# Kernel tuning notes

Hardware: AMD Instinct MI355X
Metric: run time of the kernel (lower is better)

Reference implementation:

```python
import jax, jax.numpy as jnp
import numpy as np

NUM_HEADS = 16

def setup_inputs() -> dict:
    key = jax.random.key(0)
    k1, k2, k3 = jax.random.split(key, 3)
    B, N, C = 2, 2048, 1024
    x = jax.random.normal(k1, (B, N, C), dtype=jnp.float32)
    w_qkv = jax.random.normal(k2, (C, 3 * C), dtype=jnp.float32) * (C ** -0.5)
    w_proj = jax.random.normal(k3, (C, C), dtype=jnp.float32) * (C ** -0.5)
    b_proj = jnp.zeros((C,), dtype=jnp.float32)
    return {"x": x, "w_qkv": w_qkv, "w_proj": w_proj, "b_proj": b_proj}

def reference(x, w_qkv, w_proj, b_proj):
    B, N, C = x.shape
    H = NUM_HEADS
    D = C // H
    scale = D ** -0.5
    qkv = x @ w_qkv                               # [B,N,3C]
    qkv = qkv.reshape(B, N, 3, H, D).transpose(2, 0, 3, 1, 4)  # [3,B,H,N,D]
    q, k, v = qkv[0] * scale, qkv[1], qkv[2]
    attn = jnp.einsum('bhnd,bhmd->bhnm', q, k)    # [B,H,N,N]
    attn = jax.nn.softmax(attn, axis=-1)
    out = jnp.einsum('bhnm,bhmd->bhnd', attn, v)  # [B,H,N,D]
    out = out.transpose(0, 2, 1, 3).reshape(B, N, C)
    return out @ w_proj + b_proj
```

## Files before the change

### kernel.cpp

```cpp
#include <hip/hip_runtime.h>

typedef unsigned short ushort_t;
typedef __attribute__((ext_vector_type(8))) short short8;
typedef __attribute__((ext_vector_type(4))) float f32x4;

#define AS1 __attribute__((address_space(1)))
#define AS3 __attribute__((address_space(3)))

#define EXP2F(x) __builtin_amdgcn_exp2f(x)

__device__ __forceinline__ ushort_t f2bf(float f) {
    union { float f; unsigned u; } v; v.f = f;
    unsigned r = v.u + 0x7fffu + ((v.u >> 16) & 1u);
    return (ushort_t)(r >> 16);
}

__device__ __forceinline__ unsigned pack_bf16_pair(float a, float b) {
    unsigned ua = __float_as_uint(a) + 0x8000u;
    unsigned ub = __float_as_uint(b) + 0x8000u;
    return __builtin_amdgcn_perm(ub, ua, 0x07060302u);
}

__device__ __forceinline__ void gl_lds16(const ushort_t* g, ushort_t* lds_base) {
    __builtin_amdgcn_global_load_lds((const AS1 unsigned int*)(size_t)g,
                                     (AS3 unsigned int*)lds_base, 16, 0, 0);
}

#define QSCALE 0.18033688011112042f

__device__ __forceinline__ void transpose_body(
    const float* __restrict__ in, ushort_t* __restrict__ out,
    int K0, int N0, int n, int k0)
{
    ushort_t vals[32];
#pragma unroll
    for (int kk = 0; kk < 32; kk++)
        vals[kk] = f2bf(in[(size_t)(k0 + kk) * N0 + n]);
#pragma unroll
    for (int c = 0; c < 4; c++) {
        short8 v;
#pragma unroll
        for (int e = 0; e < 8; e++) v[e] = (short)vals[c * 8 + e];
        *(short8*)&out[(size_t)n * K0 + k0 + c * 8] = v;
    }
}

__global__ __launch_bounds__(256) void prep_kernel(
    const float* __restrict__ x, const float* __restrict__ wqkv,
    const float* __restrict__ wproj,
    ushort_t* __restrict__ Xb, ushort_t* __restrict__ WqkvT,
    ushort_t* __restrict__ WpT)
{
    const int blk = blockIdx.x, t = threadIdx.x;
    if (blk < 2048) {
        int idx = (blk * 256 + t) * 8;
        float4 a = *(const float4*)&x[idx];
        float4 b = *(const float4*)&x[idx + 4];
        short8 v;
        v[0] = (short)f2bf(a.x); v[1] = (short)f2bf(a.y);
        v[2] = (short)f2bf(a.z); v[3] = (short)f2bf(a.w);
        v[4] = (short)f2bf(b.x); v[5] = (short)f2bf(b.y);
        v[6] = (short)f2bf(b.z); v[7] = (short)f2bf(b.w);
        *(short8*)&Xb[idx] = v;
    } else if (blk < 2048 + 384) {
        int i = blk - 2048;
        transpose_body(wqkv, WqkvT, 1024, 3072, (i % 12) * 256 + t, (i / 12) * 32);
    } else {
        int i = blk - 2432;
        transpose_body(wproj, WpT, 1024, 1024, (i % 4) * 256 + t, (i / 4) * 32);
    }
}

template<int JT>
__device__ __forceinline__ void mfma_gemm_core(
    const ushort_t* __restrict__ A, const ushort_t* __restrict__ Bt,
    int bm, int bn, int w, int lane,
    ushort_t* Atile, ushort_t* Btile, f32x4 acc[4][JT])
{
    const int K = 1024;
    const int wy = w >> 1, wx = w & 1;
    const int lrow8 = lane >> 3;
    const int srcoct = (lane & 7) ^ (lrow8 & 7);
    const int fr = lane & 15, fo = lane >> 4;

    for (int k0 = 0; k0 < K; k0 += 64) {
        __syncthreads();
#pragma unroll
        for (int it = 0; it < 4; it++) {
            int L = w * 4 + it;
            int r = 8 * L + lrow8;
            gl_lds16(A + (size_t)(bm + r) * K + k0 + srcoct * 8, Atile + L * 512);
        }
#pragma unroll
        for (int it = 0; it < JT; it++) {
            int L = w * JT + it;
            int r = 8 * L + lrow8;
            gl_lds16(Bt + (size_t)(bn + r) * K + k0 + srcoct * 8, Btile + L * 512);
        }
        __syncthreads();
#pragma unroll
        for (int s = 0; s < 2; s++) {
            short8 af[4], bf[JT];
#pragma unroll
            for (int i = 0; i < 4; i++) {
                int m = wy * 64 + i * 16 + fr;
                af[i] = *(const short8*)&Atile[m * 64 + (((s * 4 + fo) ^ (m & 7)) * 8)];
            }
#pragma unroll
            for (int j = 0; j < JT; j++) {
                int n = wx * (JT * 16) + j * 16 + fr;
                bf[j] = *(const short8*)&Btile[n * 64 + (((s * 4 + fo) ^ (n & 7)) * 8)];
            }
#pragma unroll
            for (int i = 0; i < 4; i++)
#pragma unroll
                for (int j = 0; j < JT; j++)
                    acc[i][j] = __builtin_amdgcn_mfma_f32_16x16x32_bf16(
                        af[i], bf[j], acc[i][j], 0, 0, 0);
        }
    }
}

__global__ __launch_bounds__(256) void qkv_gemm_kernel(
    const ushort_t* __restrict__ Xb, const ushort_t* __restrict__ WqkvT,
    ushort_t* __restrict__ Qb, ushort_t* __restrict__ Kb, ushort_t* __restrict__ Vtb)
{
    __shared__ __align__(16) ushort_t Atile[128 * 64];
    __shared__ __align__(16) ushort_t Btile[128 * 64];
    const int t = threadIdx.x, w = t >> 6, lane = t & 63;
    const int bm = blockIdx.y * 128, bn = blockIdx.x * 128;

    f32x4 acc[4][4];
#pragma unroll
    for (int i = 0; i < 4; i++)
#pragma unroll
        for (int j = 0; j < 4; j++) acc[i][j] = (f32x4){0.f, 0.f, 0.f, 0.f};

    mfma_gemm_core<4>(Xb, WqkvT, bm, bn, w, lane, Atile, Btile, acc);

    const int wy = w >> 1, wx = w & 1;
    const int colbase = bn + wx * 64 + (lane & 15);
    const int rowbase = bm + wy * 64 + (lane >> 4) * 4;
#pragma unroll
    for (int i = 0; i < 4; i++) {
        int n0 = rowbase + i * 16;
        int b = n0 >> 11, n = n0 & 2047;
#pragma unroll
        for (int j = 0; j < 4; j++) {
            int col = colbase + j * 16;
            f32x4 a = acc[i][j];
            if (col < 1024) {
                int h = col >> 6, d = col & 63;
                size_t base = ((size_t)(b * 16 + h) * 2048 + n) * 64 + d;
#pragma unroll
                for (int r = 0; r < 4; r++)
                    Qb[base + (size_t)r * 64] = f2bf(a[r] * QSCALE);
            } else if (col < 2048) {
                int hc = col & 1023;
                int h = hc >> 6, d = hc & 63;
                size_t base = ((size_t)(b * 16 + h) * 2048 + n) * 64 + d;
#pragma unroll
                for (int r = 0; r < 4; r++)
                    Kb[base + (size_t)r * 64] = f2bf(a[r]);
            } else {
                int hc = col & 1023;
                int h = hc >> 6, d = hc & 63;
                unsigned d0 = pack_bf16_pair(a[0], a[1]);
                unsigned d1 = pack_bf16_pair(a[2], a[3]);
                *(uint2*)&Vtb[((size_t)(b * 16 + h) * 64 + d) * 2048 + n] =
                    make_uint2(d0, d1);
            }
        }
    }
}

__global__ __launch_bounds__(256, 3) void attn_kernel(
    const ushort_t* __restrict__ Q, const ushort_t* __restrict__ K,
    const ushort_t* __restrict__ Vt, ushort_t* __restrict__ O)
{
    __shared__ __align__(16) ushort_t QPs[64 * 64];
    __shared__ __align__(16) ushort_t KV[2][2 * 64 * 64];
    __shared__ float l_lds[64];

    const int q0 = blockIdx.x * 64;
    const int bh = blockIdx.y;
    const int t = threadIdx.x, w = t >> 6, lane = t & 63;
    const int lrow8 = lane >> 3;
    const int srcoct = (lane & 7) ^ (lrow8 & 7);
    const int fr = lane & 15, fo = lane >> 4;

    const ushort_t* Qh = Q  + (size_t)bh * 2048 * 64;
    const ushort_t* Kh = K  + (size_t)bh * 2048 * 64;
    const ushort_t* Vh = Vt + (size_t)bh * 64 * 2048;

#pragma unroll
    for (int it = 0; it < 2; it++) {
        int L = w * 2 + it;
        int r = 16 * w + 8 * it + lrow8;
        gl_lds16(Qh + (size_t)(q0 + r) * 64 + srcoct * 8, QPs + L * 512);
        gl_lds16(Kh + (size_t)r * 64 + srcoct * 8,        &KV[0][L * 512]);
        gl_lds16(Vh + (size_t)r * 2048 + srcoct * 8,      &KV[0][4096 + L * 512]);
    }
    if (t < 64) l_lds[t] = 0.f;
    __syncthreads();

    short8 qf[4][2];
#pragma unroll
    for (int jq = 0; jq < 4; jq++)
#pragma unroll
        for (int s = 0; s < 2; s++) {
            int m = jq * 16 + fr;
            qf[jq][s] = *(const short8*)&QPs[m * 64 + (((s * 4 + fo) ^ (m & 7)) * 8)];
        }

    f32x4 o_acc[4];
    float l_part[4];
#pragma unroll
    for (int j = 0; j < 4; j++) { o_acc[j] = (f32x4){0.f, 0.f, 0.f, 0.f}; l_part[j] = 0.f; }

    int cur = 0;
    for (int kt = 0; kt < 32; kt++) {
        __syncthreads();
        const int u = (kt + 1) & 31;
        const int nxt = cur ^ 1;
#pragma unroll
        for (int it = 0; it < 2; it++) {
            int L = w * 2 + it;
            int r = 16 * w + 8 * it + lrow8;
            gl_lds16(Kh + ((size_t)u * 64 + r) * 64 + srcoct * 8, &KV[nxt][L * 512]);
            gl_lds16(Vh + (size_t)r * 2048 + u * 64 + srcoct * 8, &KV[nxt][4096 + L * 512]);
        }
        const ushort_t* Ks  = KV[cur];
        const ushort_t* Vts = KV[cur] + 4096;

        f32x4 s_acc[4];
#pragma unroll
        for (int j = 0; j < 4; j++) s_acc[j] = (f32x4){0.f, 0.f, 0.f, 0.f};
#pragma unroll
        for (int s = 0; s < 2; s++) {
            int mk = 16 * w + fr;
            short8 kf = *(const short8*)&Ks[mk * 64 + (((s * 4 + fo) ^ (mk & 7)) * 8)];
#pragma unroll
            for (int jq = 0; jq < 4; jq++)
                s_acc[jq] = __builtin_amdgcn_mfma_f32_16x16x32_bf16(
                    kf, qf[jq][s], s_acc[jq], 0, 0, 0);
        }

#pragma unroll
        for (int jq = 0; jq < 4; jq++) {
            float p0 = EXP2F(s_acc[jq][0]);
            float p1 = EXP2F(s_acc[jq][1]);
            float p2 = EXP2F(s_acc[jq][2]);
            float p3 = EXP2F(s_acc[jq][3]);
            l_part[jq] += (p0 + p1) + (p2 + p3);
            unsigned d0 = pack_bf16_pair(p0, p1);
            unsigned d1 = pack_bf16_pair(p2, p3);
            int q   = jq * 16 + fr;
            int oct = 2 * w + (fo >> 1);
            int addr = q * 64 + ((oct ^ (q & 7)) * 8) + (fo & 1) * 4;
            *(uint2*)&QPs[addr] = make_uint2(d0, d1);
        }
        __syncthreads();

#pragma unroll
        for (int s = 0; s < 2; s++) {
            int mq = 16 * w + fr;
            short8 pf = *(const short8*)&QPs[mq * 64 + (((s * 4 + fo) ^ (mq & 7)) * 8)];
#pragma unroll
            for (int jd = 0; jd < 4; jd++) {
                int nd = jd * 16 + fr;
                short8 vf = *(const short8*)&Vts[nd * 64 + (((s * 4 + fo) ^ (nd & 7)) * 8)];
                o_acc[jd] = __builtin_amdgcn_mfma_f32_16x16x32_bf16(
                    pf, vf, o_acc[jd], 0, 0, 0);
            }
        }
        cur = nxt;
    }

#pragma unroll
    for (int jq = 0; jq < 4; jq++)
        atomicAdd(&l_lds[jq * 16 + fr], l_part[jq]);
    __syncthreads();

    const int b = bh >> 4, h = bh & 15;
#pragma unroll
    for (int r = 0; r < 4; r++) {
        int qrow = 16 * w + fo * 4 + r;
        float inv = 1.f / l_lds[qrow];
        int row = b * 2048 + q0 + qrow;
#pragma unroll
        for (int jd = 0; jd < 4; jd++) {
            int col = h * 64 + jd * 16 + fr;
            O[(size_t)row * 1024 + col] = f2bf(o_acc[jd][r] * inv);
        }
    }
}

__global__ __launch_bounds__(256) void proj_gemm_kernel(
    const ushort_t* __restrict__ Ao, const ushort_t* __restrict__ WpT,
    const float* __restrict__ bias, float* __restrict__ out)
{
    __shared__ __align__(16) ushort_t Atile[128 * 64];
    __shared__ __align__(16) ushort_t Btile[64 * 64];
    const int t = threadIdx.x, w = t >> 6, lane = t & 63;
    const int bm = blockIdx.y * 128, bn = blockIdx.x * 64;

    f32x4 acc[4][2];
#pragma unroll
    for (int i = 0; i < 4; i++)
#pragma unroll
        for (int j = 0; j < 2; j++) acc[i][j] = (f32x4){0.f, 0.f, 0.f, 0.f};

    mfma_gemm_core<2>(Ao, WpT, bm, bn, w, lane, Atile, Btile, acc);

    const int wy = w >> 1, wx = w & 1;
    const int colbase = bn + wx * 32 + (lane & 15);
    const int rowbase = bm + wy * 64 + (lane >> 4) * 4;
#pragma unroll
    for (int i = 0; i < 4; i++) {
#pragma unroll
        for (int r = 0; r < 4; r++) {
            int row = rowbase + i * 16 + r;
#pragma unroll
            for (int j = 0; j < 2; j++) {
                int col = colbase + j * 16;
                out[(size_t)row * 1024 + col] = acc[i][j][r] + bias[col];
            }
        }
    }
}

extern "C" void kernel_launch(void* const* d_in, const int* in_sizes, int n_in,
                              void* d_out, int out_size, void* d_ws, size_t ws_size,
                              hipStream_t stream) {
    const float* x      = (const float*)d_in[0];
    const float* w_qkv  = (const float*)d_in[1];
    const float* w_proj = (const float*)d_in[2];
    const float* b_proj = (const float*)d_in[3];
    float* out = (float*)d_out;

    char* ws = (char*)d_ws;
    ushort_t* Xb    = (ushort_t*)(ws);
    ushort_t* WqkvT = (ushort_t*)(ws + ((size_t)8  << 20));
    ushort_t* WpT   = (ushort_t*)(ws + ((size_t)14 << 20));
    ushort_t* Qb    = (ushort_t*)(ws + ((size_t)16 << 20));
    ushort_t* Kb    = (ushort_t*)(ws + ((size_t)24 << 20));
    ushort_t* Vtb   = (ushort_t*)(ws + ((size_t)32 << 20));
    ushort_t* Aob   = (ushort_t*)(ws + ((size_t)40 << 20));

    prep_kernel<<<2560, 256, 0, stream>>>(x, w_qkv, w_proj, Xb, WqkvT, WpT);
    qkv_gemm_kernel<<<dim3(24, 32), 256, 0, stream>>>(Xb, WqkvT, Qb, Kb, Vtb);
    attn_kernel<<<dim3(32, 32), 256, 0, stream>>>(Qb, Kb, Vtb, Aob);
    proj_gemm_kernel<<<dim3(16, 32), 256, 0, stream>>>(Aob, WpT, b_proj, out);
}
```

Measured before the change: 221.9 us.

## Double attention query tile to 128 rows and drop K/V double buffering

The attention kernel now handles 128 query rows per block instead of 64. Each K/V tile loaded from global memory is therefore reused across twice as many queries, and the grid shrinks to 16x32 blocks. The K/V LDS double buffer is replaced by a single buffer that is loaded synchronously, with an extra barrier, at the start of each key tile. This gives up the overlap between the next tile's load and the current compute, and it raises register pressure, which is why occupancy is lowered to 2 blocks per SIMD-set. There are also only 512 blocks now, which may underfill the GPU.

New measurement: 202.3 us. -8.8%, faster.

```diff
diff --git a/kernel.cpp b/kernel.cpp
--- a/kernel.cpp
+++ b/kernel.cpp
@@ -174,15 +174,15 @@
     }
 }
 
-__global__ __launch_bounds__(256, 3) void attn_kernel(
+__global__ __launch_bounds__(256, 2) void attn_kernel(
     const ushort_t* __restrict__ Q, const ushort_t* __restrict__ K,
     const ushort_t* __restrict__ Vt, ushort_t* __restrict__ O)
 {
-    __shared__ __align__(16) ushort_t QPs[64 * 64];
-    __shared__ __align__(16) ushort_t KV[2][2 * 64 * 64];
-    __shared__ float l_lds[64];
-
-    const int q0 = blockIdx.x * 64;
+    __shared__ __align__(16) ushort_t QPs[128 * 64];
+    __shared__ __align__(16) ushort_t KV[2 * 64 * 64];
+    __shared__ float l_lds[128];
+
+    const int q0 = blockIdx.x * 128;
     const int bh = blockIdx.y;
     const int t = threadIdx.x, w = t >> 6, lane = t & 63;
     const int lrow8 = lane >> 3;
@@ -193,61 +193,62 @@
     const ushort_t* Kh = K  + (size_t)bh * 2048 * 64;
     const ushort_t* Vh = Vt + (size_t)bh * 64 * 2048;
 
-#pragma unroll
-    for (int it = 0; it < 2; it++) {
-        int L = w * 2 + it;
-        int r = 16 * w + 8 * it + lrow8;
+    const ushort_t* Ks  = KV;
+    const ushort_t* Vts = KV + 4096;
+
+#pragma unroll
+    for (int it = 0; it < 4; it++) {
+        int L = w * 4 + it;
+        int r = 8 * L + lrow8;
         gl_lds16(Qh + (size_t)(q0 + r) * 64 + srcoct * 8, QPs + L * 512);
-        gl_lds16(Kh + (size_t)r * 64 + srcoct * 8,        &KV[0][L * 512]);
-        gl_lds16(Vh + (size_t)r * 2048 + srcoct * 8,      &KV[0][4096 + L * 512]);
-    }
-    if (t < 64) l_lds[t] = 0.f;
+    }
+    if (t < 128) l_lds[t] = 0.f;
     __syncthreads();
 
-    short8 qf[4][2];
-#pragma unroll
-    for (int jq = 0; jq < 4; jq++)
+    short8 qf[8][2];
+#pragma unroll
+    for (int jq = 0; jq < 8; jq++)
 #pragma unroll
         for (int s = 0; s < 2; s++) {
             int m = jq * 16 + fr;
             qf[jq][s] = *(const short8*)&QPs[m * 64 + (((s * 4 + fo) ^ (m & 7)) * 8)];
         }
 
-    f32x4 o_acc[4];
-    float l_part[4];
-#pragma unroll
-    for (int j = 0; j < 4; j++) { o_acc[j] = (f32x4){0.f, 0.f, 0.f, 0.f}; l_part[j] = 0.f; }
-
-    int cur = 0;
+    f32x4 o_acc[2][4];
+    float l_part[8];
+#pragma unroll
+    for (int a = 0; a < 2; a++)
+#pragma unroll
+        for (int jd = 0; jd < 4; jd++) o_acc[a][jd] = (f32x4){0.f, 0.f, 0.f, 0.f};
+#pragma unroll
+    for (int j = 0; j < 8; j++) l_part[j] = 0.f;
+
     for (int kt = 0; kt < 32; kt++) {
         __syncthreads();
-        const int u = (kt + 1) & 31;
-        const int nxt = cur ^ 1;
 #pragma unroll
         for (int it = 0; it < 2; it++) {
             int L = w * 2 + it;
             int r = 16 * w + 8 * it + lrow8;
-            gl_lds16(Kh + ((size_t)u * 64 + r) * 64 + srcoct * 8, &KV[nxt][L * 512]);
-            gl_lds16(Vh + (size_t)r * 2048 + u * 64 + srcoct * 8, &KV[nxt][4096 + L * 512]);
-        }
-        const ushort_t* Ks  = KV[cur];
-        const ushort_t* Vts = KV[cur] + 4096;
-
-        f32x4 s_acc[4];
-#pragma unroll
-        for (int j = 0; j < 4; j++) s_acc[j] = (f32x4){0.f, 0.f, 0.f, 0.f};
+            gl_lds16(Kh + ((size_t)kt * 64 + r) * 64 + srcoct * 8, (ushort_t*)Ks + L * 512);
+            gl_lds16(Vh + (size_t)r * 2048 + kt * 64 + srcoct * 8, (ushort_t*)Vts + L * 512);
+        }
+        __syncthreads();
+
+        f32x4 s_acc[8];
+#pragma unroll
+        for (int j = 0; j < 8; j++) s_acc[j] = (f32x4){0.f, 0.f, 0.f, 0.f};
 #pragma unroll
         for (int s = 0; s < 2; s++) {
             int mk = 16 * w + fr;
             short8 kf = *(const short8*)&Ks[mk * 64 + (((s * 4 + fo) ^ (mk & 7)) * 8)];
 #pragma unroll
-            for (int jq = 0; jq < 4; jq++)
+            for (int jq = 0; jq < 8; jq++)
                 s_acc[jq] = __builtin_amdgcn_mfma_f32_16x16x32_bf16(
                     kf, qf[jq][s], s_acc[jq], 0, 0, 0);
         }
 
 #pragma unroll
-        for (int jq = 0; jq < 4; jq++) {
+        for (int jq = 0; jq < 8; jq++) {
             float p0 = EXP2F(s_acc[jq][0]);
             float p1 = EXP2F(s_acc[jq][1]);
             float p2 = EXP2F(s_acc[jq][2]);
@@ -264,36 +265,43 @@
 
 #pragma unroll
         for (int s = 0; s < 2; s++) {
-            int mq = 16 * w + fr;
-            short8 pf = *(const short8*)&QPs[mq * 64 + (((s * 4 + fo) ^ (mq & 7)) * 8)];
+            short8 pf[2];
+#pragma unroll
+            for (int a = 0; a < 2; a++) {
+                int mq = 32 * w + 16 * a + fr;
+                pf[a] = *(const short8*)&QPs[mq * 64 + (((s * 4 + fo) ^ (mq & 7)) * 8)];
+            }
 #pragma unroll
             for (int jd = 0; jd < 4; jd++) {
                 int nd = jd * 16 + fr;
                 short8 vf = *(const short8*)&Vts[nd * 64 + (((s * 4 + fo) ^ (nd & 7)) * 8)];
-                o_acc[jd] = __builtin_amdgcn_mfma_f32_16x16x32_bf16(
-                    pf, vf, o_acc[jd], 0, 0, 0);
-            }
-        }
-        cur = nxt;
-    }
-
-#pragma unroll
-    for (int jq = 0; jq < 4; jq++)
+#pragma unroll
+                for (int a = 0; a < 2; a++)
+                    o_acc[a][jd] = __builtin_amdgcn_mfma_f32_16x16x32_bf16(
+                        pf[a], vf, o_acc[a][jd], 0, 0, 0);
+            }
+        }
+    }
+
+#pragma unroll
+    for (int jq = 0; jq < 8; jq++)
         atomicAdd(&l_lds[jq * 16 + fr], l_part[jq]);
     __syncthreads();
 
     const int b = bh >> 4, h = bh & 15;
 #pragma unroll
-    for (int r = 0; r < 4; r++) {
-        int qrow = 16 * w + fo * 4 + r;
-        float inv = 1.f / l_lds[qrow];
-        int row = b * 2048 + q0 + qrow;
-#pragma unroll
-        for (int jd = 0; jd < 4; jd++) {
-            int col = h * 64 + jd * 16 + fr;
-            O[(size_t)row * 1024 + col] = f2bf(o_acc[jd][r] * inv);
-        }
-    }
+    for (int a = 0; a < 2; a++)
+#pragma unroll
+        for (int r = 0; r < 4; r++) {
+            int qrow = 32 * w + 16 * a + fo * 4 + r;
+            float inv = 1.f / l_lds[qrow];
+            int row = b * 2048 + q0 + qrow;
+#pragma unroll
+            for (int jd = 0; jd < 4; jd++) {
+                int col = h * 64 + jd * 16 + fr;
+                O[(size_t)row * 1024 + col] = f2bf(o_acc[a][jd][r] * inv);
+            }
+        }
 }
 
 __global__ __launch_bounds__(256) void proj_gemm_kernel(
@@ -350,6 +358,6 @@
 
     prep_kernel<<<2560, 256, 0, stream>>>(x, w_qkv, w_proj, Xb, WqkvT, WpT);
     qkv_gemm_kernel<<<dim3(24, 32), 256, 0, stream>>>(Xb, WqkvT, Qb, Kb, Vtb);
-    attn_kernel<<<dim3(32, 32), 256, 0, stream>>>(Qb, Kb, Vtb, Aob);
+    attn_kernel<<<dim3(16, 32), 256, 0, stream>>>(Qb, Kb, Vtb, Aob);
     proj_gemm_kernel<<<dim3(16, 32), 256, 0, stream>>>(Aob, WpT, b_proj, out);
 }
```
